# Kernel tuning notes

Hardware: AMD Instinct MI355X
Metric: run time of the kernel (lower is better)

Reference implementation:

```python
import jax, jax.numpy as jnp
import numpy as np

N = 100000  # nodes
E = 1600000  # edges
D_IN, D_HID, D_OUT = 128, 128, 64
NEG_SLOPE = 0.2


def gat_conv(x, src, dst, W_src, W_dst, att_src, att_dst, bias, num_nodes):
    # PyG GATConv, heads=1, add_self_loops=False.
    h_src = x @ W_src          # [N, C]
    h_dst = x @ W_dst          # [N, C]
    a_src = (h_src * att_src).sum(-1)   # [N]
    a_dst = (h_dst * att_dst).sum(-1)   # [N]
    logits = jax.nn.leaky_relu(a_src[src] + a_dst[dst], NEG_SLOPE)  # [E]
    # segment softmax over destination neighborhoods
    seg_max = jax.ops.segment_max(logits, dst, num_segments=num_nodes)  # [N]
    e = jnp.exp(logits - seg_max[dst])
    denom = jax.ops.segment_sum(e, dst, num_segments=num_nodes)         # [N]
    alpha = e / (denom[dst] + 1e-16)                                    # [E]
    out = jax.ops.segment_sum(alpha[:, None] * h_src[src], dst, num_segments=num_nodes)  # [N, C]
    return out + bias


def setup_inputs() -> dict:
    key = jax.random.key(0)
    ks = jax.random.split(key, 12)
    x = jax.random.normal(ks[0], (N, D_IN), dtype=jnp.float32)
    edge_index = jax.random.randint(ks[1], (2, E), 0, N, dtype=jnp.int64)
    s1 = 1.0 / np.sqrt(D_IN)
    s2 = 1.0 / np.sqrt(D_HID)
    return {
        "x": x,
        "edge_index": edge_index,
        "W1_src": jax.random.uniform(ks[2], (D_IN, D_HID), jnp.float32, -s1, s1),
        "W1_dst": jax.random.uniform(ks[3], (D_IN, D_HID), jnp.float32, -s1, s1),
        "att1_src": jax.random.uniform(ks[4], (D_HID,), jnp.float32, -s2, s2),
        "att1_dst": jax.random.uniform(ks[5], (D_HID,), jnp.float32, -s2, s2),
        "b1": jnp.zeros((D_HID,), jnp.float32),
        "W2_src": jax.random.uniform(ks[6], (D_HID, D_OUT), jnp.float32, -s2, s2),
        "W2_dst": jax.random.uniform(ks[7], (D_HID, D_OUT), jnp.float32, -s2, s2),
        "att2_src": jax.random.uniform(ks[8], (D_OUT,), jnp.float32, -1.0 / np.sqrt(D_OUT), 1.0 / np.sqrt(D_OUT)),
        "att2_dst": jax.random.uniform(ks[9], (D_OUT,), jnp.float32, -1.0 / np.sqrt(D_OUT), 1.0 / np.sqrt(D_OUT)),
        "b2": jnp.zeros((D_OUT,), jnp.float32),
    }


def reference(x, edge_index, W1_src, W1_dst, att1_src, att1_dst, b1,
              W2_src, W2_dst, att2_src, att2_dst, b2):
    src, dst = edge_index[0], edge_index[1]
    h = gat_conv(x, src, dst, W1_src, W1_dst, att1_src, att1_dst, b1, N)
    h = jax.nn.relu(h)
    out = gat_conv(h, src, dst, W2_src, W2_dst, att2_src, att2_dst, b2, N)
    return out
```

## Files before the change

kernel.cpp:

```cpp
#include <hip/hip_runtime.h>


typedef unsigned long long u64;
typedef float v4f __attribute__((ext_vector_type(4)));
typedef _Float16 v2h __attribute__((ext_vector_type(2)));
typedef __fp16 h8 __attribute__((ext_vector_type(8)));

#define SEL_LO 0x01000504u
#define SEL_HI 0x03020706u

__device__ __forceinline__ void ntstore4(float* p, v4f v) {
    __builtin_nontemporal_store(v, (v4f*)p);
}
__device__ __forceinline__ unsigned h2pack(float a, float b) {
    v2h h;
    h.x = (_Float16)a;
    h.y = (_Float16)b;
    return __builtin_bit_cast(unsigned, h);
}
__device__ __forceinline__ float fdot2u(unsigned u, v2h w, float acc) {
    return __builtin_amdgcn_fdot2(__builtin_bit_cast(v2h, u), w, acc, false);
}
__device__ __forceinline__ v2h pkrtz(float a, float b) {
    return __builtin_bit_cast(v2h, __builtin_amdgcn_cvt_pkrtz(a, b));
}

__global__ __launch_bounds__(64) void matvec_kernel(const float* __restrict__ W,
                                                    const float* __restrict__ a,
                                                    float* __restrict__ out, int cols) {
    int row = blockIdx.x;
    int lane = threadIdx.x;
    float s = 0.f;
    for (int j = lane; j < cols; j += 64) s += W[row * cols + j] * a[j];
#pragma unroll
    for (int o = 32; o; o >>= 1) s += __shfl_xor(s, o, 64);
    if (lane == 0) out[row] = s;
}

template <int C>
__global__ __launch_bounds__(256) void packw_kernel(const float* __restrict__ W,
                                                    uint4* __restrict__ Wp) {
    constexpr int NT = C / 16;
    const int total = 4 * NT * 64;
    for (int e = threadIdx.x; e < total; e += 256) {
        int lane = e & 63;
        int ti = (e >> 6) % NT;
        int t = (e >> 6) / NT;
        int k0 = 32 * t + (lane >> 4) * 8;
        int n = ti * 16 + (lane & 15);
        unsigned u[4];
#pragma unroll
        for (int p = 0; p < 4; ++p)
            u[p] = h2pack(W[(size_t)(k0 + 2 * p) * C + n], W[(size_t)(k0 + 2 * p + 1) * C + n]);
        Wp[e] = make_uint4(u[0], u[1], u[2], u[3]);
    }
}

__global__ __launch_bounds__(256) void bhist_kernel(const int* __restrict__ dst,
                                                    int* __restrict__ gh, int E) {
    __shared__ int h[256];
    h[threadIdx.x] = 0;
    __syncthreads();
    int base = blockIdx.x * 4096;
    int lim = min(base + 4096, E);
    for (int i = base + threadIdx.x; i < lim; i += 256)
        atomicAdd(&h[__builtin_nontemporal_load(dst + i) >> 9], 1);
    __syncthreads();
    int v = h[threadIdx.x];
    if (v) atomicAdd(&gh[threadIdx.x], v);
}

__global__ __launch_bounds__(256) void bscan_kernel(const int* __restrict__ gh,
                                                    int* __restrict__ bbase,
                                                    int* __restrict__ gcur,
                                                    int* __restrict__ offs, int N, int E) {
    __shared__ int s[256];
    int t = threadIdx.x;
    int v = gh[t];
    s[t] = v;
    __syncthreads();
    for (int o = 1; o < 256; o <<= 1) {
        int u = (t >= o) ? s[t - o] : 0;
        __syncthreads();
        s[t] += u;
        __syncthreads();
    }
    int excl = s[t] - v;
    bbase[t] = excl;
    gcur[t] = excl;
    if (t == 255) { bbase[256] = E; offs[N] = E; }
}

__global__ __launch_bounds__(256) void bscatter_kernel(const int* __restrict__ src,
                                                       const int* __restrict__ dst,
                                                       int* __restrict__ gcur,
                                                       u64* __restrict__ pairs, int E) {
    __shared__ int h[256];
    __shared__ int rbase[256];
    const int tid = threadIdx.x;
    h[tid] = 0;
    __syncthreads();
    const int base = blockIdx.x * 4096;
    u64 pv[16];
    int rk[16];
    int bk[16];
#pragma unroll 16
    for (int k = 0; k < 16; ++k) {
        int i = base + k * 256 + tid;
        if (i < E) {
            int d = __builtin_nontemporal_load(dst + i);
            int b = d >> 9;
            bk[k] = b;
            pv[k] = ((u64)(unsigned)d << 32) | (unsigned)__builtin_nontemporal_load(src + i);
            rk[k] = atomicAdd(&h[b], 1);
        } else {
            bk[k] = -1;
        }
    }
    __syncthreads();
    int c = h[tid];
    rbase[tid] = c ? atomicAdd(&gcur[tid], c) : 0;
    __syncthreads();
#pragma unroll 16
    for (int k = 0; k < 16; ++k)
        if (bk[k] >= 0)
            __builtin_nontemporal_store(pv[k], pairs + (size_t)rbase[bk[k]] + rk[k]);
}

__global__ __launch_bounds__(512) void bsort_kernel(const u64* __restrict__ pairs,
                                                    const int* __restrict__ bbase,
                                                    int* __restrict__ offs,
                                                    int* __restrict__ srcs, int N) {
    __shared__ int h[512];
    __shared__ int cur[512];
    const int t = threadIdx.x;
    const int b = blockIdx.x;
    const int beg = bbase[b], end = bbase[b + 1];
    h[t] = 0;
    __syncthreads();
    for (int i = beg + t; i < end; i += 512)
        atomicAdd(&h[(int)(__builtin_nontemporal_load(pairs + i) >> 32) & 511], 1);
    __syncthreads();
    int v = h[t];
    cur[t] = v;
    __syncthreads();
    for (int o = 1; o < 512; o <<= 1) {
        int u = (t >= o) ? cur[t - o] : 0;
        __syncthreads();
        cur[t] += u;
        __syncthreads();
    }
    int pos0 = beg + cur[t] - v;
    __syncthreads();
    cur[t] = pos0;
    int g = (b << 9) + t;
    if (g < N) offs[g] = pos0;
    __syncthreads();
    for (int i = beg + t; i < end; i += 512) {
        u64 p = __builtin_nontemporal_load(pairs + i);
        int local = (int)(p >> 32) & 511;
        int pp = atomicAdd(&cur[local], 1);
        srcs[pp] = (int)(p & 0xffffffffu);
    }
}

template <int C, bool XF16>
__global__ __launch_bounds__(256) void gemm_att_kernel(
    const void* __restrict__ Xv, const uint4* __restrict__ Wp,
    const float* __restrict__ attS, const float* __restrict__ wda,
    unsigned* __restrict__ H, float* __restrict__ aS, float* __restrict__ aD, int M) {
    constexpr int NT = C / 16;
    __shared__ _Float16 hs[4][16 * 136];

    const int tid = threadIdx.x;
    const int w = tid >> 6;
    const int lane = tid & 63;
    const int l15 = lane & 15;
    const int q = lane >> 4;
    const int mb = blockIdx.x * 64 + w * 16;
    const int m = mb + l15;
    const bool mv = m < M;

    v4f acc[NT];
#pragma unroll
    for (int n = 0; n < NT; ++n) acc[n] = (v4f)(0.f);
    float pd = 0.f;
    uint4 afu[4];

    if constexpr (XF16) {
        const uint4* Xp = (const uint4*)Xv + (size_t)m * 16;
#pragma unroll
        for (int t = 0; t < 4; ++t) {
            uint4 u = make_uint4(0u, 0u, 0u, 0u);
            if (mv) u = Xp[4 * t + q];
            afu[t] = u;
            const float* wdp = wda + 32 * t + 8 * q;
            pd = fdot2u(u.x, pkrtz(wdp[0], wdp[1]), pd);
            pd = fdot2u(u.y, pkrtz(wdp[2], wdp[3]), pd);
            pd = fdot2u(u.z, pkrtz(wdp[4], wdp[5]), pd);
            pd = fdot2u(u.w, pkrtz(wdp[6], wdp[7]), pd);
        }
    } else {
        const float* Xp = (const float*)Xv + (size_t)m * 128;
#pragma unroll
        for (int t = 0; t < 4; ++t) {
            float4 x0 = make_float4(0.f, 0.f, 0.f, 0.f);
            float4 x1 = x0;
            if (mv) {
                x0 = *(const float4*)(Xp + 32 * t + 8 * q);
                x1 = *(const float4*)(Xp + 32 * t + 8 * q + 4);
            }
            const float* wdp = wda + 32 * t + 8 * q;
            pd += x0.x * wdp[0] + x0.y * wdp[1] + x0.z * wdp[2] + x0.w * wdp[3] +
                  x1.x * wdp[4] + x1.y * wdp[5] + x1.z * wdp[6] + x1.w * wdp[7];
            afu[t] = make_uint4(h2pack(x0.x, x0.y), h2pack(x0.z, x0.w),
                                h2pack(x1.x, x1.y), h2pack(x1.z, x1.w));
        }
    }

#pragma unroll
    for (int t = 0; t < 4; ++t) {
        h8 a = __builtin_bit_cast(h8, afu[t]);
        const uint4* wp = Wp + (size_t)t * NT * 64 + lane;
#pragma unroll
        for (int n = 0; n < NT; ++n) {
            h8 b = __builtin_bit_cast(h8, wp[n * 64]);
            acc[n] = __builtin_amdgcn_mfma_f32_16x16x32_f16(a, b, acc[n], 0, 0, 0);
        }
    }

    pd += __shfl_xor(pd, 16, 64);
    pd += __shfl_xor(pd, 32, 64);
    if (q == 0 && mv) aD[m] = pd;

    float as4[4] = {0.f, 0.f, 0.f, 0.f};
#pragma unroll
    for (int n = 0; n < NT; ++n) {
        float av = attS[n * 16 + l15];
#pragma unroll
        for (int r = 0; r < 4; ++r) as4[r] += acc[n][r] * av;
    }
#pragma unroll
    for (int r = 0; r < 4; ++r) {
#pragma unroll
        for (int o = 1; o < 16; o <<= 1) as4[r] += __shfl_xor(as4[r], o, 64);
    }
    if (l15 == 0) {
#pragma unroll
        for (int r = 0; r < 4; ++r) {
            int row = mb + q * 4 + r;
            if (row < M) aS[row] = as4[r];
        }
    }

    _Float16* hp = hs[w];
#pragma unroll
    for (int n = 0; n < NT; ++n)
#pragma unroll
        for (int r = 0; r < 4; ++r)
            hp[(q * 4 + r) * 136 + n * 16 + l15] = (_Float16)acc[n][r];

    constexpr int CH = C / 32;
    if (lane < 16 * CH) {
        int row = lane / CH;
        int ch = lane % CH;
        const uint4* rp = (const uint4*)(hp + row * 136 + ch * 32);
        uint4 v0 = rp[0], v1 = rp[1], v2 = rp[2], v3 = rp[3];
        int gr = mb + row;
        if (gr < M) {
            uint4* op = (uint4*)(H + (size_t)gr * (C / 2)) + ch * 4;
            op[0] = v0; op[1] = v1; op[2] = v2; op[3] = v3;
        }
    }
}

template <int C, bool RELU, bool F16OUT, bool NTOUT>
__global__ __launch_bounds__(256) void aggregate_kernel(
    const int* __restrict__ offs, const int* __restrict__ srcs,
    const unsigned* __restrict__ hsrc, const float* __restrict__ aS,
    const float* __restrict__ aD, const float* __restrict__ bias,
    void* __restrict__ outv, int n) {
    int node = (int)((blockIdx.x * blockDim.x + threadIdx.x) >> 6);
    int lane = threadIdx.x & 63;
    if (node >= n) return;
    int beg = offs[node], end = offs[node + 1];
    int deg = end - beg;
    float ad = aD[node];
    const int g = lane >> 4;
    const int l = lane & 15;

    constexpr int NA = C / 16;
    float acc[NA];
#pragma unroll
    for (int i = 0; i < NA; ++i) acc[i] = 0.f;

    auto quad = [&](float wv, int sj, int j) {
        int e0 = (j + 0) * 4 + g, e1 = (j + 1) * 4 + g;
        int e2 = (j + 2) * 4 + g, e3 = (j + 3) * 4 + g;
        float w0 = __shfl(wv, e0, 64), w1 = __shfl(wv, e1, 64);
        float w2 = __shfl(wv, e2, 64), w3 = __shfl(wv, e3, 64);
        int s0 = __shfl(sj, e0, 64), s1 = __shfl(sj, e1, 64);
        int s2 = __shfl(sj, e2, 64), s3 = __shfl(sj, e3, 64);
        v2h w01 = pkrtz(w0, w1);
        v2h w23 = pkrtz(w2, w3);
        if constexpr (C == 128) {
            uint4 a = ((const uint4*)(hsrc + ((size_t)s0 << 6)))[l];
            uint4 b = ((const uint4*)(hsrc + ((size_t)s1 << 6)))[l];
            uint4 c = ((const uint4*)(hsrc + ((size_t)s2 << 6)))[l];
            uint4 d = ((const uint4*)(hsrc + ((size_t)s3 << 6)))[l];
            const unsigned* au = (const unsigned*)&a;
            const unsigned* bu = (const unsigned*)&b;
            const unsigned* cu = (const unsigned*)&c;
            const unsigned* du = (const unsigned*)&d;
#pragma unroll
            for (int i = 0; i < 4; ++i) {
                acc[2 * i] = fdot2u(__builtin_amdgcn_perm(au[i], bu[i], SEL_LO), w01,
                             fdot2u(__builtin_amdgcn_perm(cu[i], du[i], SEL_LO), w23, acc[2 * i]));
                acc[2 * i + 1] = fdot2u(__builtin_amdgcn_perm(au[i], bu[i], SEL_HI), w01,
                                 fdot2u(__builtin_amdgcn_perm(cu[i], du[i], SEL_HI), w23, acc[2 * i + 1]));
            }
        } else {
            uint2 a = ((const uint2*)(hsrc + ((size_t)s0 << 5)))[l];
            uint2 b = ((const uint2*)(hsrc + ((size_t)s1 << 5)))[l];
            uint2 c = ((const uint2*)(hsrc + ((size_t)s2 << 5)))[l];
            uint2 d = ((const uint2*)(hsrc + ((size_t)s3 << 5)))[l];
            const unsigned* au = (const unsigned*)&a;
            const unsigned* bu = (const unsigned*)&b;
            const unsigned* cu = (const unsigned*)&c;
            const unsigned* du = (const unsigned*)&d;
#pragma unroll
            for (int i = 0; i < 2; ++i) {
                acc[2 * i] = fdot2u(__builtin_amdgcn_perm(au[i], bu[i], SEL_LO), w01,
                             fdot2u(__builtin_amdgcn_perm(cu[i], du[i], SEL_LO), w23, acc[2 * i]));
                acc[2 * i + 1] = fdot2u(__builtin_amdgcn_perm(au[i], bu[i], SEL_HI), w01,
                                 fdot2u(__builtin_amdgcn_perm(cu[i], du[i], SEL_HI), w23, acc[2 * i + 1]));
            }
        }
    };

    if (deg <= 64) {
        int i = beg + lane;
        int sj = 0;
        float w = 0.f;
        if (i < end) {
            sj = __builtin_nontemporal_load(srcs + i);
            float lg = aS[sj] + ad;
            lg = (lg > 0.f) ? lg : 0.2f * lg;
            w = __expf(lg);
        }
        float s = w;
#pragma unroll
        for (int o = 32; o; o >>= 1) s += __shfl_xor(s, o, 64);
        w *= 1.f / (s + 1e-16f);
        int jm = (deg + 3) >> 2;
        for (int j = 0; j < jm; j += 4) quad(w, sj, j);
    } else {
        float m = -INFINITY;
        for (int i = beg + lane; i < end; i += 64) {
            float lg = aS[srcs[i]] + ad;
            lg = (lg > 0.f) ? lg : 0.2f * lg;
            m = fmaxf(m, lg);
        }
#pragma unroll
        for (int o = 32; o; o >>= 1) m = fmaxf(m, __shfl_xor(m, o, 64));
        float s = 0.f;
        for (int i = beg + lane; i < end; i += 64) {
            float lg = aS[srcs[i]] + ad;
            lg = (lg > 0.f) ? lg : 0.2f * lg;
            s += __expf(lg - m);
        }
#pragma unroll
        for (int o = 32; o; o >>= 1) s += __shfl_xor(s, o, 64);
        float inv = 1.f / (s + 1e-16f);
        for (int base = beg; base < end; base += 64) {
            int i = base + lane;
            int sj = 0;
            float w = 0.f;
            if (i < end) {
                sj = srcs[i];
                float lg = aS[sj] + ad;
                lg = (lg > 0.f) ? lg : 0.2f * lg;
                w = __expf(lg - m) * inv;
            }
            int cnt = min(64, end - base);
            int jm = (cnt + 3) >> 2;
            for (int j = 0; j < jm; j += 4) quad(w, sj, j);
        }
    }

#pragma unroll
    for (int i = 0; i < NA; ++i) {
        acc[i] += __shfl_xor(acc[i], 16, 64);
        acc[i] += __shfl_xor(acc[i], 32, 64);
    }

    if (lane < 16) {
        float o[NA];
        const float* bp = bias + lane * NA;
#pragma unroll
        for (int i = 0; i < NA; ++i) {
            o[i] = acc[i] + bp[i];
            if (RELU) o[i] = fmaxf(o[i], 0.f);
        }
        if constexpr (F16OUT) {
            unsigned u[NA / 2];
#pragma unroll
            for (int k = 0; k < NA / 2; ++k) u[k] = h2pack(o[2 * k], o[2 * k + 1]);
            unsigned* op = (unsigned*)outv + (size_t)node * (C / 2) + lane * (NA / 2);
            if constexpr (NA == 8) *(uint4*)op = make_uint4(u[0], u[1], u[2], u[3]);
            else *(uint2*)op = make_uint2(u[0], u[1]);
        } else {
            float* op = (float*)outv + (size_t)node * C + lane * NA;
#pragma unroll
            for (int q = 0; q < NA / 4; ++q) {
                v4f ov;
                ov.x = o[q * 4 + 0]; ov.y = o[q * 4 + 1];
                ov.z = o[q * 4 + 2]; ov.w = o[q * 4 + 3];
                if (NTOUT) ntstore4(op + q * 4, ov);
                else *(v4f*)(op + q * 4) = ov;
            }
        }
    }
}

extern "C" void kernel_launch(void* const* d_in, const int* in_sizes, int n_in,
                              void* d_out, int out_size, void* d_ws, size_t ws_size,
                              hipStream_t stream) {
    const float* x     = (const float*)d_in[0];
    const int*   edge  = (const int*)d_in[1];
    const float* W1s   = (const float*)d_in[2];
    const float* W1d   = (const float*)d_in[3];
    const float* att1s = (const float*)d_in[4];
    const float* att1d = (const float*)d_in[5];
    const float* b1    = (const float*)d_in[6];
    const float* W2s   = (const float*)d_in[7];
    const float* W2d   = (const float*)d_in[8];
    const float* att2s = (const float*)d_in[9];
    const float* att2d = (const float*)d_in[10];
    const float* b2    = (const float*)d_in[11];

    const int N = in_sizes[0] / 128;
    const int E = in_sizes[1] / 2;
    const int* srcI = edge;
    const int* dstI = edge + E;

    size_t off = 0;
    auto alloc = [&](size_t bytes) {
        void* p = (char*)d_ws + off;
        off += (bytes + 255) & ~(size_t)255;
        return p;
    };
    int*      offs  = (int*)alloc((size_t)(N + 1) * 4);
    int*      srcs  = (int*)alloc((size_t)E * 4);
    int*      gh    = (int*)alloc(256 * 4);
    int*      bbase = (int*)alloc(257 * 4);
    int*      gcur  = (int*)alloc(256 * 4);
    float*    watt1 = (float*)alloc(128 * 4);
    float*    watt2 = (float*)alloc(128 * 4);
    uint4*    wp1   = (uint4*)alloc(4 * 8 * 64 * 16);
    uint4*    wp2   = (uint4*)alloc(4 * 4 * 64 * 16);
    float*    a_s   = (float*)alloc((size_t)N * 4);
    float*    a_d   = (float*)alloc((size_t)N * 4);
    unsigned* g1h   = (unsigned*)alloc((size_t)N * 128 * 2);
    unsigned* h1h   = (unsigned*)alloc((size_t)N * 128 * 2);
    unsigned* g2h   = (unsigned*)alloc((size_t)N * 64 * 2);
    u64*      pairs = (u64*)h1h;

    hipMemsetAsync(gh, 0, 256 * 4, stream);
    matvec_kernel<<<128, 64, 0, stream>>>(W1d, att1d, watt1, 128);
    matvec_kernel<<<128, 64, 0, stream>>>(W2d, att2d, watt2, 64);
    packw_kernel<128><<<1, 256, 0, stream>>>(W1s, wp1);
    packw_kernel<64><<<1, 256, 0, stream>>>(W2s, wp2);

    const int nbE = (E + 4095) / 4096;
    const int nbuckets = (N + 511) >> 9;
    bhist_kernel<<<nbE, 256, 0, stream>>>(dstI, gh, E);
    bscan_kernel<<<1, 256, 0, stream>>>(gh, bbase, gcur, offs, N, E);
    bscatter_kernel<<<nbE, 256, 0, stream>>>(srcI, dstI, gcur, pairs, E);
    bsort_kernel<<<nbuckets, 512, 0, stream>>>(pairs, bbase, offs, srcs, N);

    int gblk = (N + 63) / 64;
    gemm_att_kernel<128, false><<<gblk, 256, 0, stream>>>(x, wp1, att1s, watt1, g1h, a_s, a_d, N);
    aggregate_kernel<128, true, true, false><<<(N + 3) / 4, 256, 0, stream>>>(
        offs, srcs, g1h, a_s, a_d, b1, h1h, N);
    gemm_att_kernel<64, true><<<gblk, 256, 0, stream>>>(h1h, wp2, att2s, watt2, g2h, a_s, a_d, N);
    aggregate_kernel<64, false, false, true><<<(N + 3) / 4, 256, 0, stream>>>(
        offs, srcs, g2h, a_s, a_d, b2, d_out, N);
}
```

Measured before the change: 335.6 us.

## Assign half-wavefront per node in aggregation with double-buffered row loads

The aggregation kernel now maps each destination node to 32 lanes instead of a full 64-lane wavefront, so each wave handles two nodes and the grid is halved. Neighbor row gathers are issued into two alternating register buffers before the softmax normalizer is reduced, so memory loads overlap the reduction and the dot-product compute. Weights are now scaled by the inverse sum at compute time instead of beforehand. The fast path now covers degrees up to 32, so nodes with degree 33 to 64 take the three-pass max/sum route. The extra buffers also raise register use.

```diff
diff --git a/kernel.cpp b/kernel.cpp
--- a/kernel.cpp
+++ b/kernel.cpp
@@ -280,137 +280,142 @@
     const unsigned* __restrict__ hsrc, const float* __restrict__ aS,
     const float* __restrict__ aD, const float* __restrict__ bias,
     void* __restrict__ outv, int n) {
-    int node = (int)((blockIdx.x * blockDim.x + threadIdx.x) >> 6);
-    int lane = threadIdx.x & 63;
+    const int lane = threadIdx.x & 63;
+    const int sl = lane & 31;
+    const int hb = lane & 32;
+    const int g = (lane >> 4) & 1;
+    const int l = lane & 15;
+    int node = (int)((blockIdx.x * blockDim.x + threadIdx.x) >> 5);
     if (node >= n) return;
-    int beg = offs[node], end = offs[node + 1];
-    int deg = end - beg;
-    float ad = aD[node];
-    const int g = lane >> 4;
-    const int l = lane & 15;
-
+
+    const int beg = offs[node], end = offs[node + 1];
+    const int deg = end - beg;
+    const float ad = aD[node];
+
+    constexpr int LW = C / 32;
     constexpr int NA = C / 16;
     float acc[NA];
 #pragma unroll
     for (int i = 0; i < NA; ++i) acc[i] = 0.f;
 
-    auto quad = [&](float wv, int sj, int j) {
-        int e0 = (j + 0) * 4 + g, e1 = (j + 1) * 4 + g;
-        int e2 = (j + 2) * 4 + g, e3 = (j + 3) * 4 + g;
-        float w0 = __shfl(wv, e0, 64), w1 = __shfl(wv, e1, 64);
-        float w2 = __shfl(wv, e2, 64), w3 = __shfl(wv, e3, 64);
-        int s0 = __shfl(sj, e0, 64), s1 = __shfl(sj, e1, 64);
-        int s2 = __shfl(sj, e2, 64), s3 = __shfl(sj, e3, 64);
+    int sj = 0;
+    float u = 0.f;
+
+    auto ldrow = [&](int s, unsigned* r) {
+        if constexpr (C == 128) {
+            uint4 v = ((const uint4*)(hsrc + ((size_t)s << 6)))[l];
+            r[0] = v.x; r[1] = v.y; r[2] = v.z; r[3] = v.w;
+        } else {
+            uint2 v = ((const uint2*)(hsrc + ((size_t)s << 5)))[l];
+            r[0] = v.x; r[1] = v.y;
+        }
+    };
+    auto issue = [&](int j, unsigned (*buf)[LW]) {
+        int e0 = hb + j * 8 + g;
+        int s0 = __shfl(sj, e0, 64);
+        int s1 = __shfl(sj, e0 + 2, 64);
+        int s2 = __shfl(sj, e0 + 4, 64);
+        int s3 = __shfl(sj, e0 + 6, 64);
+        ldrow(s0, buf[0]);
+        ldrow(s1, buf[1]);
+        ldrow(s2, buf[2]);
+        ldrow(s3, buf[3]);
+    };
+    auto compute = [&](int j, unsigned (*buf)[LW], float inv) {
+        int e0 = hb + j * 8 + g;
+        float w0 = __shfl(u, e0, 64) * inv, w1 = __shfl(u, e0 + 2, 64) * inv;
+        float w2 = __shfl(u, e0 + 4, 64) * inv, w3 = __shfl(u, e0 + 6, 64) * inv;
         v2h w01 = pkrtz(w0, w1);
         v2h w23 = pkrtz(w2, w3);
-        if constexpr (C == 128) {
-            uint4 a = ((const uint4*)(hsrc + ((size_t)s0 << 6)))[l];
-            uint4 b = ((const uint4*)(hsrc + ((size_t)s1 << 6)))[l];
-            uint4 c = ((const uint4*)(hsrc + ((size_t)s2 << 6)))[l];
-            uint4 d = ((const uint4*)(hsrc + ((size_t)s3 << 6)))[l];
-            const unsigned* au = (const unsigned*)&a;
-            const unsigned* bu = (const unsigned*)&b;
-            const unsigned* cu = (const unsigned*)&c;
-            const unsigned* du = (const unsigned*)&d;
-#pragma unroll
-            for (int i = 0; i < 4; ++i) {
-                acc[2 * i] = fdot2u(__builtin_amdgcn_perm(au[i], bu[i], SEL_LO), w01,
-                             fdot2u(__builtin_amdgcn_perm(cu[i], du[i], SEL_LO), w23, acc[2 * i]));
-                acc[2 * i + 1] = fdot2u(__builtin_amdgcn_perm(au[i], bu[i], SEL_HI), w01,
-                                 fdot2u(__builtin_amdgcn_perm(cu[i], du[i], SEL_HI), w23, acc[2 * i + 1]));
-            }
-        } else {
-            uint2 a = ((const uint2*)(hsrc + ((size_t)s0 << 5)))[l];
-            uint2 b = ((const uint2*)(hsrc + ((size_t)s1 << 5)))[l];
-            uint2 c = ((const uint2*)(hsrc + ((size_t)s2 << 5)))[l];
-            uint2 d = ((const uint2*)(hsrc + ((size_t)s3 << 5)))[l];
-            const unsigned* au = (const unsigned*)&a;
-            const unsigned* bu = (const unsigned*)&b;
-            const unsigned* cu = (const unsigned*)&c;
-            const unsigned* du = (const unsigned*)&d;
-#pragma unroll
-            for (int i = 0; i < 2; ++i) {
-                acc[2 * i] = fdot2u(__builtin_amdgcn_perm(au[i], bu[i], SEL_LO), w01,
-                             fdot2u(__builtin_amdgcn_perm(cu[i], du[i], SEL_LO), w23, acc[2 * i]));
-                acc[2 * i + 1] = fdot2u(__builtin_amdgcn_perm(au[i], bu[i], SEL_HI), w01,
-                                 fdot2u(__builtin_amdgcn_perm(cu[i], du[i], SEL_HI), w23, acc[2 * i + 1]));
-            }
+#pragma unroll
+        for (int ii = 0; ii < LW; ++ii) {
+            acc[2 * ii] = fdot2u(__builtin_amdgcn_perm(buf[0][ii], buf[1][ii], SEL_LO), w01,
+                          fdot2u(__builtin_amdgcn_perm(buf[2][ii], buf[3][ii], SEL_LO), w23, acc[2 * ii]));
+            acc[2 * ii + 1] = fdot2u(__builtin_amdgcn_perm(buf[0][ii], buf[1][ii], SEL_HI), w01,
+                              fdot2u(__builtin_amdgcn_perm(buf[2][ii], buf[3][ii], SEL_HI), w23, acc[2 * ii + 1]));
         }
     };
 
-    if (deg <= 64) {
-        int i = beg + lane;
-        int sj = 0;
-        float w = 0.f;
+    unsigned A0[4][LW], A1[4][LW];
+
+    if (deg <= 32) {
+        int i = beg + sl;
         if (i < end) {
             sj = __builtin_nontemporal_load(srcs + i);
             float lg = aS[sj] + ad;
             lg = (lg > 0.f) ? lg : 0.2f * lg;
-            w = __expf(lg);
-        }
-        float s = w;
-#pragma unroll
-        for (int o = 32; o; o >>= 1) s += __shfl_xor(s, o, 64);
-        w *= 1.f / (s + 1e-16f);
-        int jm = (deg + 3) >> 2;
-        for (int j = 0; j < jm; j += 4) quad(w, sj, j);
+            u = __expf(lg);
+        }
+        int jm = (deg + 7) >> 3;
+        if (jm > 0) issue(0, A0);
+        if (jm > 1) issue(1, A1);
+        float s = u;
+#pragma unroll
+        for (int o = 16; o; o >>= 1) s += __shfl_xor(s, o, 64);
+        float inv = 1.f / (s + 1e-16f);
+        if (jm > 0) { compute(0, A0, inv); if (jm > 2) issue(2, A0); }
+        if (jm > 1) { compute(1, A1, inv); if (jm > 3) issue(3, A1); }
+        if (jm > 2) compute(2, A0, inv);
+        if (jm > 3) compute(3, A1, inv);
     } else {
         float m = -INFINITY;
-        for (int i = beg + lane; i < end; i += 64) {
+        for (int i = beg + sl; i < end; i += 32) {
             float lg = aS[srcs[i]] + ad;
             lg = (lg > 0.f) ? lg : 0.2f * lg;
             m = fmaxf(m, lg);
         }
 #pragma unroll
-        for (int o = 32; o; o >>= 1) m = fmaxf(m, __shfl_xor(m, o, 64));
-        float s = 0.f;
-        for (int i = beg + lane; i < end; i += 64) {
+        for (int o = 16; o; o >>= 1) m = fmaxf(m, __shfl_xor(m, o, 64));
+        float ssum = 0.f;
+        for (int i = beg + sl; i < end; i += 32) {
             float lg = aS[srcs[i]] + ad;
             lg = (lg > 0.f) ? lg : 0.2f * lg;
-            s += __expf(lg - m);
-        }
-#pragma unroll
-        for (int o = 32; o; o >>= 1) s += __shfl_xor(s, o, 64);
-        float inv = 1.f / (s + 1e-16f);
-        for (int base = beg; base < end; base += 64) {
-            int i = base + lane;
-            int sj = 0;
-            float w = 0.f;
+            ssum += __expf(lg - m);
+        }
+#pragma unroll
+        for (int o = 16; o; o >>= 1) ssum += __shfl_xor(ssum, o, 64);
+        float inv = 1.f / (ssum + 1e-16f);
+        for (int base = beg; base < end; base += 32) {
+            int i = base + sl;
+            sj = 0;
+            u = 0.f;
             if (i < end) {
                 sj = srcs[i];
                 float lg = aS[sj] + ad;
                 lg = (lg > 0.f) ? lg : 0.2f * lg;
-                w = __expf(lg - m) * inv;
+                u = __expf(lg - m);
             }
-            int cnt = min(64, end - base);
-            int jm = (cnt + 3) >> 2;
-            for (int j = 0; j < jm; j += 4) quad(w, sj, j);
-        }
-    }
-
-#pragma unroll
-    for (int i = 0; i < NA; ++i) {
-        acc[i] += __shfl_xor(acc[i], 16, 64);
-        acc[i] += __shfl_xor(acc[i], 32, 64);
-    }
-
-    if (lane < 16) {
+            int cnt = min(32, end - base);
+            int cj = (cnt + 7) >> 3;
+            if (cj > 0) issue(0, A0);
+            if (cj > 1) issue(1, A1);
+            if (cj > 0) { compute(0, A0, inv); if (cj > 2) issue(2, A0); }
+            if (cj > 1) { compute(1, A1, inv); if (cj > 3) issue(3, A1); }
+            if (cj > 2) compute(2, A0, inv);
+            if (cj > 3) compute(3, A1, inv);
+        }
+    }
+
+#pragma unroll
+    for (int i = 0; i < NA; ++i) acc[i] += __shfl_xor(acc[i], 16, 64);
+
+    if (sl < 16) {
         float o[NA];
-        const float* bp = bias + lane * NA;
+        const float* bp = bias + l * NA;
 #pragma unroll
         for (int i = 0; i < NA; ++i) {
             o[i] = acc[i] + bp[i];
             if (RELU) o[i] = fmaxf(o[i], 0.f);
         }
         if constexpr (F16OUT) {
-            unsigned u[NA / 2];
-#pragma unroll
-            for (int k = 0; k < NA / 2; ++k) u[k] = h2pack(o[2 * k], o[2 * k + 1]);
-            unsigned* op = (unsigned*)outv + (size_t)node * (C / 2) + lane * (NA / 2);
-            if constexpr (NA == 8) *(uint4*)op = make_uint4(u[0], u[1], u[2], u[3]);
-            else *(uint2*)op = make_uint2(u[0], u[1]);
+            unsigned uo[NA / 2];
+#pragma unroll
+            for (int k = 0; k < NA / 2; ++k) uo[k] = h2pack(o[2 * k], o[2 * k + 1]);
+            unsigned* op = (unsigned*)outv + (size_t)node * (C / 2) + l * (NA / 2);
+            if constexpr (NA == 8) *(uint4*)op = make_uint4(uo[0], uo[1], uo[2], uo[3]);
+            else *(uint2*)op = make_uint2(uo[0], uo[1]);
         } else {
-            float* op = (float*)outv + (size_t)node * C + lane * NA;
+            float* op = (float*)outv + (size_t)node * C + l * NA;
 #pragma unroll
             for (int q = 0; q < NA / 4; ++q) {
                 v4f ov;
@@ -481,9 +486,9 @@
 
     int gblk = (N + 63) / 64;
     gemm_att_kernel<128, false><<<gblk, 256, 0, stream>>>(x, wp1, att1s, watt1, g1h, a_s, a_d, N);
-    aggregate_kernel<128, true, true, false><<<(N + 3) / 4, 256, 0, stream>>>(
+    aggregate_kernel<128, true, true, false><<<(N + 7) / 8, 256, 0, stream>>>(
         offs, srcs, g1h, a_s, a_d, b1, h1h, N);
     gemm_att_kernel<64, true><<<gblk, 256, 0, stream>>>(h1h, wp2, att2s, watt2, g2h, a_s, a_d, N);
-    aggregate_kernel<64, false, false, true><<<(N + 3) / 4, 256, 0, stream>>>(
+    aggregate_kernel<64, false, false, true><<<(N + 7) / 8, 256, 0, stream>>>(
         offs, srcs, g2h, a_s, a_d, b2, d_out, N);
 }
```

Measured after the change: 327.4 us. -2.4%, faster.
